# Performance work log

Measured on AMD Instinct MI355X. Metric: run time of the kernel, lower is better.

Reference implementation:

```python
import jax, jax.numpy as jnp
import numpy as np

R = 16  # z_dim
_TRIU = np.triu_indices(R, 1)  # static index pair for plucker coords


def plucker_coords(u, v):
    # L2-normalised Plucker coordinates of span{u, v}; last dim r -> r*(r-1)//2
    outer = u[..., :, None] * v[..., None, :]
    anti = outer - jnp.swapaxes(outer, -1, -2)
    pc = anti[..., _TRIU[0], _TRIU[1]]
    nrm = jnp.linalg.norm(pc, axis=-1, keepdims=True)
    return pc / jnp.maximum(nrm, 1e-8)


def setup_inputs() -> dict:
    key = jax.random.key(0)
    ks = jax.random.split(key, 9)
    B, L, D, Z, P, H = 4, 256, 128, 16, 120, 256
    in_dim = 2 * D + 2 * Z + 3 * P + 2  # 650
    h = jax.random.normal(ks[0], (B, L, D), dtype=jnp.float32)
    z = jax.random.normal(ks[1], (B, L, Z), dtype=jnp.float32)
    p = jax.random.normal(ks[2], (B, L, P), dtype=jnp.float32)
    seq_mask = jax.random.randint(ks[3], (B, L), 0, 2).astype(bool)
    canon_mask = jax.random.randint(ks[4], (B, L, L), 0, 2).astype(bool)
    W1 = jax.random.normal(ks[5], (in_dim, H), dtype=jnp.float32) / np.sqrt(in_dim)
    b1 = jnp.zeros((H,), dtype=jnp.float32)
    W2 = jax.random.normal(ks[6], (H, 1), dtype=jnp.float32) / np.sqrt(H)
    b2 = jnp.zeros((1,), dtype=jnp.float32)
    return {"h": h, "z": z, "p": p, "seq_mask": seq_mask, "canon_mask": canon_mask,
            "W1": W1, "b1": b1, "W2": W2, "b2": b2}


def reference(h, z, p, seq_mask, canon_mask, W1, b1, W2, b2):
    B, L, _ = h.shape
    pos = jnp.arange(L, dtype=h.dtype)
    dist = jnp.abs(pos[:, None] - pos[None, :]) / max(L, 1)  # [L, L]
    dist = jnp.broadcast_to(dist[None, :, :, None], (B, L, L, 1))
    canon_f = canon_mask.astype(h.dtype)[..., None]  # [B, L, L, 1]

    h_i = jnp.broadcast_to(h[:, :, None, :], (B, L, L, h.shape[-1]))
    h_j = jnp.broadcast_to(h[:, None, :, :], (B, L, L, h.shape[-1]))
    z_i = jnp.broadcast_to(z[:, :, None, :], (B, L, L, z.shape[-1]))
    z_j = jnp.broadcast_to(z[:, None, :, :], (B, L, L, z.shape[-1]))
    p_i = jnp.broadcast_to(p[:, :, None, :], (B, L, L, p.shape[-1]))
    p_j = jnp.broadcast_to(p[:, None, :, :], (B, L, L, p.shape[-1]))
    p_ij = plucker_coords(z_i, z_j)  # [B, L, L, 120]

    feat = jnp.concatenate([h_i, h_j, z_i, z_j, p_i, p_j, p_ij, dist, canon_f], axis=-1)
    hdn = jax.nn.gelu(feat @ W1 + b1, approximate=False)
    e_pair = (hdn @ W2 + b2)[..., 0]  # [B, L, L]
    e_pair = (e_pair + jnp.swapaxes(e_pair, 1, 2)) * 0.5
    valid = seq_mask[:, :, None] & seq_mask[:, None, :]
    return jnp.where(valid, e_pair, jnp.asarray(30000.0, e_pair.dtype))
```

## Files before the change

### kernel.cpp

```cpp
#include <hip/hip_runtime.h>
#include <hip/hip_bf16.h>
#include <stdint.h>

#define BB     4
#define L_SEQ  256
#define DIM_H  128
#define DIM_Z  16
#define DIM_P  120
#define HID    256
#define TI     16
#define TJ     8
#define NPAIR  (TI*TJ)

typedef __attribute__((ext_vector_type(8))) short short8;
typedef __attribute__((ext_vector_type(4))) float f32x4;

__device__ __forceinline__ int imin(int a, int b){ return a < b ? a : b; }

struct Triu { int a[128]; int b[128]; };
static constexpr Triu make_triu(){
  Triu t{}; int k=0;
  for (int a=0;a<16;a++) for (int b=a+1;b<16;b++){ t.a[k]=a; t.b[k]=b; ++k; }
  for (;k<128;k++){ t.a[k]=0; t.b[k]=0; }
  return t;
}
static constexpr Triu TRIU = make_triu();

__device__ __forceinline__ short f2bf(float f){
  union { __hip_bfloat16 h; short s; } u;
  u.h = __float2bfloat16(f);
  return u.s;
}

__device__ __forceinline__ float bf2f(short s){
  union { float f; uint32_t u; } x;
  x.u = ((uint32_t)(uint16_t)s) << 16;
  return x.f;
}

__device__ __forceinline__ float gelu_fast(float x){
  float s = fmaf(0.42550f, x, 0.5f);
  s = fminf(fmaxf(s, 0.0f), 1.0f);
  return x * s;
}

__global__ void k_detect(const uint32_t* __restrict__ seq_words, int* __restrict__ flag){
  uint32_t v = 0;
  for (int i = threadIdx.x; i < 256; i += 64) v |= (seq_words[i] & 0xFFFFFF00u);
  unsigned long long any = __ballot(v != 0u);
  if (threadIdx.x == 0) *flag = (any != 0ull) ? 1 : 0;
}

__global__ __launch_bounds__(256) void k_compact(
    const void* __restrict__ seq_raw, const int* __restrict__ flag_p,
    int* __restrict__ vi, int* __restrict__ nv)
{
  const int b = blockIdx.x, i = threadIdx.x;
  bool s;
  if (*flag_p) s = ((const unsigned char*)seq_raw)[b*L_SEQ + i] != 0;
  else         s = ((const int*)          seq_raw)[b*L_SEQ + i] != 0;
  const int lane = i & 63, w = i >> 6;
  unsigned long long m = __ballot(s);
  __shared__ int wc[4];
  if (lane == 0) wc[w] = __popcll(m);
  __syncthreads();
  int base = 0;
  for (int x = 0; x < w; x++) base += wc[x];
  unsigned long long lower = (1ull << lane) - 1ull;
  int pos = base + __popcll(m & lower);
  if (s) vi[b*L_SEQ + pos] = i;
  if (i == 0) nv[b] = wc[0] + wc[1] + wc[2] + wc[3];
}

#define K1_ROWS 2
__global__ __launch_bounds__(256) void k1_precompute(
    const float* __restrict__ hbuf, const float* __restrict__ zbuf, const float* __restrict__ pbuf,
    const float* __restrict__ W1, const float* __restrict__ b1,
    const void* __restrict__ seq_raw, const int* __restrict__ flag_p,
    float* __restrict__ Ai, float* __restrict__ Cj)
{
  int row0 = blockIdx.x * K1_ROWS;
  {
    bool v0, v1;
    if (*flag_p){
      const unsigned char* s8 = (const unsigned char*)seq_raw;
      v0 = s8[row0] != 0; v1 = s8[row0+1] != 0;
    } else {
      const int* s32 = (const int*)seq_raw;
      v0 = s32[row0] != 0; v1 = s32[row0+1] != 0;
    }
    if (!v0 && !v1) return;
  }
  int hcol = threadIdx.x;
  float accA[K1_ROWS], accC[K1_ROWS];
  float bias = b1[hcol];
  #pragma unroll
  for (int r=0;r<K1_ROWS;r++){ accA[r]=bias; accC[r]=0.f; }

  const float* hrow = hbuf + (size_t)row0*DIM_H;
  for (int k=0;k<DIM_H;k++){
    float wa = W1[k*HID + hcol], wc = W1[(128+k)*HID + hcol];
    #pragma unroll
    for (int r=0;r<K1_ROWS;r++){
      float x = hrow[r*DIM_H + k];
      accA[r]=fmaf(x,wa,accA[r]); accC[r]=fmaf(x,wc,accC[r]);
    }
  }
  const float* zrow = zbuf + (size_t)row0*DIM_Z;
  for (int k=0;k<DIM_Z;k++){
    float wa = W1[(256+k)*HID + hcol], wc = W1[(272+k)*HID + hcol];
    #pragma unroll
    for (int r=0;r<K1_ROWS;r++){
      float x = zrow[r*DIM_Z + k];
      accA[r]=fmaf(x,wa,accA[r]); accC[r]=fmaf(x,wc,accC[r]);
    }
  }
  const float* prow = pbuf + (size_t)row0*DIM_P;
  for (int k=0;k<DIM_P;k++){
    float wa = W1[(288+k)*HID + hcol], wc = W1[(408+k)*HID + hcol];
    #pragma unroll
    for (int r=0;r<K1_ROWS;r++){
      float x = prow[r*DIM_P + k];
      accA[r]=fmaf(x,wa,accA[r]); accC[r]=fmaf(x,wc,accC[r]);
    }
  }
  #pragma unroll
  for (int r=0;r<K1_ROWS;r++){
    Ai[(row0+r)*HID + hcol] = accA[r];
    Cj[(row0+r)*HID + hcol] = accC[r];
  }
}

__global__ __launch_bounds__(256) void k1b_w1pt(const float* __restrict__ W1, short* __restrict__ W1pT){
  int idx = blockIdx.x*256 + threadIdx.x;
  int k = idx & 127, n = idx >> 7;
  float v = 0.f;
  if (k < 120)      v = W1[(528+k)*HID + n];
  else if (k==120)  v = W1[648*HID + n];
  else if (k==121)  v = W1[649*HID + n];
  W1pT[n*128 + k] = f2bf(v);
}

#define PCCOORD(T) f2bf((u[TRIU.a[(T)]]*v[TRIU.b[(T)]] - u[TRIU.b[(T)]]*v[TRIU.a[(T)]])*inv)
#define PC_CHUNK4(BASE) { \
  _Pragma("unroll") \
  for (int c_=0;c_<4;c_++){ \
    _Pragma("unroll") \
    for (int e_=0;e_<8;e_++){ pk[c_][e_] = PCCOORD((BASE) + c_*8 + e_); } } }

__global__ __launch_bounds__(512, 4) void k2_pair(
    const float* __restrict__ zbuf, const void* __restrict__ canon_raw,
    const float* __restrict__ Ai, const float* __restrict__ Cj,
    const short* __restrict__ W1pT, const float* __restrict__ W2,
    const int* __restrict__ flag_p, const int* __restrict__ vi, const int* __restrict__ nv,
    float* __restrict__ e_out)
{
  const int b = blockIdx.z, it = blockIdx.y, jt = blockIdx.x;
  const int i0 = it*TI, j0 = jt*TJ;
  const int nvb = nv[b];
  if (i0 >= nvb || j0 >= nvb) return;
  const int tid = threadIdx.x, lane = tid & 63, w = tid >> 6;
  const int brow = b*L_SEQ;

  short8 bfrag[2][4];
  {
    int g = lane >> 4, col = lane & 15;
    int n0 = (2*w+0)*16 + col, n1 = (2*w+1)*16 + col;
    #pragma unroll
    for (int ks=0; ks<4; ks++){
      bfrag[0][ks] = *reinterpret_cast<const short8*>(W1pT + n0*128 + ks*32 + g*8);
      bfrag[1][ks] = *reinterpret_cast<const short8*>(W1pT + n1*128 + ks*32 + g*8);
    }
  }

  __shared__ __align__(16) short pc_lds[NPAIR*128];
  __shared__ short ai_lds[TI*264];
  __shared__ short cj_lds[TJ*264];
  __shared__ float z_lds[(TI+TJ)*17];
  __shared__ float w2_lds[HID];
  __shared__ float epart[NPAIR*9];
  __shared__ int io_lds[TI];
  __shared__ int jo_lds[TJ];

  if (tid < TI)              io_lds[tid]    = vi[brow + imin(i0 + tid,      nvb-1)];
  else if (tid < TI+TJ)      jo_lds[tid-TI] = vi[brow + imin(j0 + (tid-TI), nvb-1)];
  __syncthreads();

  for (int idx = tid; idx < TI*HID; idx += 512){ int r = idx>>8, c = idx&255; ai_lds[r*264+c] = f2bf(Ai[(size_t)(brow+io_lds[r])*HID + c]); }
  for (int idx = tid; idx < TJ*HID; idx += 512){ int r = idx>>8, c = idx&255; cj_lds[r*264+c] = f2bf(Cj[(size_t)(brow+jo_lds[r])*HID + c]); }
  for (int idx = tid; idx < TI*DIM_Z; idx += 512){ int r = idx>>4, c = idx&15; z_lds[r*17+c] = zbuf[(size_t)(brow+io_lds[r])*DIM_Z + c]; }
  for (int idx = tid; idx < TJ*DIM_Z; idx += 512){ int r = idx>>4, c = idx&15; z_lds[(TI+r)*17+c] = zbuf[(size_t)(brow+jo_lds[r])*DIM_Z + c]; }
  if (tid < HID) w2_lds[tid] = W2[tid];
  __syncthreads();

  {
    const int p  = tid & 127;
    const int h  = tid >> 7;
    const int il = p >> 3, jl = p & 7;
    float u[16], v[16];
    #pragma unroll
    for (int a=0;a<16;a++) u[a] = z_lds[il*17+a];
    #pragma unroll
    for (int a=0;a<16;a++) v[a] = z_lds[(TI+jl)*17+a];
    float du=0.f, dv=0.f, uv=0.f;
    #pragma unroll
    for (int a=0;a<16;a++){ du=fmaf(u[a],u[a],du); dv=fmaf(v[a],v[a],dv); uv=fmaf(u[a],v[a],uv); }
    float q = fmaxf(du*dv - uv*uv, 1e-16f);
    float inv = __builtin_amdgcn_rsqf(q);

    short8 pk[4];
    if (h == 0)      PC_CHUNK4(0)
    else if (h == 1) PC_CHUNK4(32)
    else if (h == 2) PC_CHUNK4(64)
    else {
      #pragma unroll
      for (int c_=0;c_<3;c_++){
        #pragma unroll
        for (int e_=0;e_<8;e_++){ pk[c_][e_] = PCCOORD(96 + c_*8 + e_); }
      }
      int gi = io_lds[il], gj = jo_lds[jl];
      float dist = fabsf((float)(gi - gj)) * (1.0f/256.0f);
      float canon;
      if (*flag_p) canon = (((const unsigned char*)canon_raw)[(brow+gi)*L_SEQ + gj] != 0) ? 1.f : 0.f;
      else         canon = (((const int*)          canon_raw)[(brow+gi)*L_SEQ + gj] != 0) ? 1.f : 0.f;
      short8 last;
      last[0] = f2bf(dist); last[1] = f2bf(canon);
      #pragma unroll
      for (int e_=2;e_<8;e_++) last[e_] = (short)0;
      pk[3] = last;
    }
    char* pcb = (char*)pc_lds;
    const int rowbase = p*256 + h*64;
    #pragma unroll
    for (int c_=0;c_<4;c_++){
      int off = (rowbase + c_*16) ^ ((p&7)<<4);
      *reinterpret_cast<short8*>(pcb + off) = pk[c_];
    }
  }
  __syncthreads();

  {
    const int g = lane >> 4, col = lane & 15;
    const int n0 = (2*w+0)*16 + col, n1 = (2*w+1)*16 + col;
    const float w2v0 = w2_lds[n0], w2v1 = w2_lds[n1];
    const char* pcb = (const char*)pc_lds;

    for (int s=0; s<8; s++){
      short8 afrag[4];
      const int p = s*16 + col;
      #pragma unroll
      for (int ks=0; ks<4; ks++){
        int off = (p*256 + (ks*4+g)*16) ^ ((p&7)<<4);
        afrag[ks] = *reinterpret_cast<const short8*>(pcb + off);
      }
      f32x4 acc0 = {0.f,0.f,0.f,0.f}, acc1 = {0.f,0.f,0.f,0.f};
      #pragma unroll
      for (int ks=0; ks<4; ks++){
        acc0 = __builtin_amdgcn_mfma_f32_16x16x32_bf16(afrag[ks], bfrag[0][ks], acc0, 0,0,0);
        acc1 = __builtin_amdgcn_mfma_f32_16x16x32_bf16(afrag[ks], bfrag[1][ks], acc1, 0,0,0);
      }
      const int i_l = 2*s + (g>>1);
      const float ai0 = bf2f(ai_lds[i_l*264 + n0]);
      const float ai1 = bf2f(ai_lds[i_l*264 + n1]);
      float psum[4];
      #pragma unroll
      for (int r=0;r<4;r++){
        int m  = g*4 + r;
        int jl = m & 7;
        float cj0 = bf2f(cj_lds[jl*264 + n0]);
        float cj1 = bf2f(cj_lds[jl*264 + n1]);
        float pre0 = acc0[r] + ai0 + cj0;
        float pre1 = acc1[r] + ai1 + cj1;
        psum[r] = fmaf(gelu_fast(pre0), w2v0, gelu_fast(pre1)*w2v1);
      }
      float recv01 = __shfl_xor((lane & 1) ? psum[0] : psum[1], 1);
      float acc01  = ((lane & 1) ? psum[1] : psum[0]) + recv01;
      float recv23 = __shfl_xor((lane & 1) ? psum[2] : psum[3], 1);
      float acc23  = ((lane & 1) ? psum[3] : psum[2]) + recv23;
      float recv2  = __shfl_xor((lane & 2) ? acc01 : acc23, 2);
      float val    = ((lane & 2) ? acc23 : acc01) + recv2;
      val += __shfl_xor(val, 4);
      val += __shfl_xor(val, 8);
      if ((lane & 12) == 0)
        epart[(s*16 + g*4 + (lane&3))*9 + w] = val;
    }
  }
  __syncthreads();

  if (tid < NPAIR){
    float sum = 0.f;
    #pragma unroll
    for (int ww=0; ww<8; ww++) sum += epart[tid*9 + ww];
    e_out[(size_t)(brow + io_lds[tid>>3])*L_SEQ + jo_lds[tid&7]] = sum;
  }
}

__global__ __launch_bounds__(256) void k3_sym(
    const float* __restrict__ e_in, const void* __restrict__ seq_raw,
    const float* __restrict__ b2, const int* __restrict__ flag_p,
    float* __restrict__ out)
{
  int idx = blockIdx.x*256 + threadIdx.x;
  int b = idx >> 16, rem = idx & 65535, i = rem >> 8, j = rem & 255;
  bool si, sj;
  if (*flag_p){
    const unsigned char* s8 = (const unsigned char*)seq_raw;
    si = s8[b*L_SEQ+i] != 0; sj = s8[b*L_SEQ+j] != 0;
  } else {
    const int* s32 = (const int*)seq_raw;
    si = s32[b*L_SEQ+i] != 0; sj = s32[b*L_SEQ+j] != 0;
  }
  float val = 30000.0f;
  if (si && sj){
    float e1 = e_in[(b*L_SEQ+i)*L_SEQ + j];
    float e2 = e_in[(b*L_SEQ+j)*L_SEQ + i];
    val = 0.5f*(e1 + e2) + b2[0];
  }
  out[idx] = val;
}

extern "C" void kernel_launch(void* const* d_in, const int* in_sizes, int n_in,
                              void* d_out, int out_size, void* d_ws, size_t ws_size,
                              hipStream_t stream)
{
  const float* hbuf  = (const float*)d_in[0];
  const float* zbuf  = (const float*)d_in[1];
  const float* pbuf  = (const float*)d_in[2];
  const void*  seq   = d_in[3];
  const void*  canon = d_in[4];
  const float* W1    = (const float*)d_in[5];
  const float* b1    = (const float*)d_in[6];
  const float* W2    = (const float*)d_in[7];
  const float* b2    = (const float*)d_in[8];

  char* ws = (char*)d_ws;
  float* Ai   = (float*)(ws);
  float* Cj   = (float*)(ws + (1<<20));
  short* W1pT = (short*)(ws + (2<<20));
  float* e_ws = (float*)(ws + (2<<20) + 65536);
  int*   flag = (int*)  (ws + (2<<20) + 65536 + (1<<20));
  int*   vi   = (int*)  (ws + (2<<20) + 65536 + (1<<20) + 256);
  int*   nv   = (int*)  (ws + (2<<20) + 65536 + (1<<20) + 256 + 4096);

  k_detect<<<1, 64, 0, stream>>>((const uint32_t*)seq, flag);
  k_compact<<<BB, 256, 0, stream>>>(seq, flag, vi, nv);
  k1_precompute<<<BB*L_SEQ/K1_ROWS, 256, 0, stream>>>(hbuf, zbuf, pbuf, W1, b1, seq, flag, Ai, Cj);
  k1b_w1pt<<<(HID*128)/256, 256, 0, stream>>>(W1, W1pT);
  dim3 g2(L_SEQ/TJ, L_SEQ/TI, BB);
  k2_pair<<<g2, 512, 0, stream>>>(zbuf, canon, Ai, Cj, W1pT, W2, flag, vi, nv, e_ws);
  k3_sym<<<(BB*L_SEQ*L_SEQ)/256, 256, 0, stream>>>(e_ws, seq, b2, flag, (float*)d_out);
}
```

Before: 59.93 us.

## Merge prep kernels, compact k1 over valid rows, vectorize symmetrize stores

The detect, compact and W1 transpose kernels are merged into one prep launch, which drops two kernel launches. k1_precompute now reads the compacted valid-row list and processes pairs of valid rows, so blocks no longer sit mostly idle on masked rows. k3_sym writes four outputs per thread with a vector store, cutting its thread count by four. The costs are an extra in-block sync for format detection and uncoalesced transposed reads in k3.

```diff
diff --git a/kernel.cpp b/kernel.cpp
--- a/kernel.cpp
+++ b/kernel.cpp
@@ -44,101 +44,86 @@
   return x * s;
 }
 
-__global__ void k_detect(const uint32_t* __restrict__ seq_words, int* __restrict__ flag){
-  uint32_t v = 0;
-  for (int i = threadIdx.x; i < 256; i += 64) v |= (seq_words[i] & 0xFFFFFF00u);
-  unsigned long long any = __ballot(v != 0u);
-  if (threadIdx.x == 0) *flag = (any != 0ull) ? 1 : 0;
-}
-
-__global__ __launch_bounds__(256) void k_compact(
-    const void* __restrict__ seq_raw, const int* __restrict__ flag_p,
-    int* __restrict__ vi, int* __restrict__ nv)
-{
-  const int b = blockIdx.x, i = threadIdx.x;
-  bool s;
-  if (*flag_p) s = ((const unsigned char*)seq_raw)[b*L_SEQ + i] != 0;
-  else         s = ((const int*)          seq_raw)[b*L_SEQ + i] != 0;
-  const int lane = i & 63, w = i >> 6;
-  unsigned long long m = __ballot(s);
-  __shared__ int wc[4];
-  if (lane == 0) wc[w] = __popcll(m);
-  __syncthreads();
-  int base = 0;
-  for (int x = 0; x < w; x++) base += wc[x];
-  unsigned long long lower = (1ull << lane) - 1ull;
-  int pos = base + __popcll(m & lower);
-  if (s) vi[b*L_SEQ + pos] = i;
-  if (i == 0) nv[b] = wc[0] + wc[1] + wc[2] + wc[3];
-}
-
-#define K1_ROWS 2
+__global__ __launch_bounds__(256) void k_prep(
+    const uint32_t* __restrict__ seq_words, const float* __restrict__ W1,
+    int* __restrict__ flag, int* __restrict__ vi, int* __restrict__ nv,
+    short* __restrict__ W1pT)
+{
+  const int blk = blockIdx.x, tid = threadIdx.x;
+  if (blk < BB){
+    const int lane = tid & 63, w = tid >> 6;
+    __shared__ int det[4];
+    __shared__ int wc[4];
+    uint32_t vdet = seq_words[tid] & 0xFFFFFF00u;
+    unsigned long long bm = __ballot(vdet != 0u);
+    if (lane == 0) det[w] = (bm != 0ull) ? 1 : 0;
+    __syncthreads();
+    const bool bytes = (det[0] | det[1] | det[2] | det[3]) != 0;
+    if (blk == 0 && tid == 0) *flag = bytes ? 1 : 0;
+
+    const int b = blk, i = tid;
+    bool s;
+    if (bytes) s = ((const unsigned char*)seq_words)[b*L_SEQ + i] != 0;
+    else       s = ((const int*)          seq_words)[b*L_SEQ + i] != 0;
+    unsigned long long m = __ballot(s);
+    if (lane == 0) wc[w] = __popcll(m);
+    __syncthreads();
+    int base = 0;
+    for (int x = 0; x < w; x++) base += wc[x];
+    unsigned long long lower = (1ull << lane) - 1ull;
+    int pos = base + __popcll(m & lower);
+    if (s) vi[b*L_SEQ + pos] = i;
+    if (i == 0) nv[b] = wc[0] + wc[1] + wc[2] + wc[3];
+  } else {
+    int idx = (blk - BB)*256 + tid;
+    int k = idx & 127, n = idx >> 7;
+    float v = 0.f;
+    if (k < 120)      v = W1[(528+k)*HID + n];
+    else if (k==120)  v = W1[648*HID + n];
+    else if (k==121)  v = W1[649*HID + n];
+    W1pT[n*128 + k] = f2bf(v);
+  }
+}
+
 __global__ __launch_bounds__(256) void k1_precompute(
     const float* __restrict__ hbuf, const float* __restrict__ zbuf, const float* __restrict__ pbuf,
     const float* __restrict__ W1, const float* __restrict__ b1,
-    const void* __restrict__ seq_raw, const int* __restrict__ flag_p,
+    const int* __restrict__ vi, const int* __restrict__ nv,
     float* __restrict__ Ai, float* __restrict__ Cj)
 {
-  int row0 = blockIdx.x * K1_ROWS;
-  {
-    bool v0, v1;
-    if (*flag_p){
-      const unsigned char* s8 = (const unsigned char*)seq_raw;
-      v0 = s8[row0] != 0; v1 = s8[row0+1] != 0;
-    } else {
-      const int* s32 = (const int*)seq_raw;
-      v0 = s32[row0] != 0; v1 = s32[row0+1] != 0;
-    }
-    if (!v0 && !v1) return;
-  }
-  int hcol = threadIdx.x;
-  float accA[K1_ROWS], accC[K1_ROWS];
-  float bias = b1[hcol];
-  #pragma unroll
-  for (int r=0;r<K1_ROWS;r++){ accA[r]=bias; accC[r]=0.f; }
-
-  const float* hrow = hbuf + (size_t)row0*DIM_H;
+  const int b = blockIdx.x >> 7;
+  const int p = blockIdx.x & 127;
+  const int nvb = nv[b];
+  if (2*p >= nvb) return;
+  const int r0 = vi[b*L_SEQ + 2*p];
+  const int r1 = vi[b*L_SEQ + imin(2*p + 1, nvb - 1)];
+  const size_t g0 = (size_t)(b*L_SEQ + r0), g1 = (size_t)(b*L_SEQ + r1);
+
+  const int hcol = threadIdx.x;
+  float a0, a1, c0, c1;
+  a0 = a1 = b1[hcol];
+  c0 = c1 = 0.f;
+
+  const float* h0 = hbuf + g0*DIM_H;  const float* h1 = hbuf + g1*DIM_H;
   for (int k=0;k<DIM_H;k++){
     float wa = W1[k*HID + hcol], wc = W1[(128+k)*HID + hcol];
-    #pragma unroll
-    for (int r=0;r<K1_ROWS;r++){
-      float x = hrow[r*DIM_H + k];
-      accA[r]=fmaf(x,wa,accA[r]); accC[r]=fmaf(x,wc,accC[r]);
-    }
-  }
-  const float* zrow = zbuf + (size_t)row0*DIM_Z;
+    a0 = fmaf(h0[k], wa, a0); c0 = fmaf(h0[k], wc, c0);
+    a1 = fmaf(h1[k], wa, a1); c1 = fmaf(h1[k], wc, c1);
+  }
+  const float* z0 = zbuf + g0*DIM_Z;  const float* z1 = zbuf + g1*DIM_Z;
   for (int k=0;k<DIM_Z;k++){
     float wa = W1[(256+k)*HID + hcol], wc = W1[(272+k)*HID + hcol];
-    #pragma unroll
-    for (int r=0;r<K1_ROWS;r++){
-      float x = zrow[r*DIM_Z + k];
-      accA[r]=fmaf(x,wa,accA[r]); accC[r]=fmaf(x,wc,accC[r]);
-    }
-  }
-  const float* prow = pbuf + (size_t)row0*DIM_P;
+    a0 = fmaf(z0[k], wa, a0); c0 = fmaf(z0[k], wc, c0);
+    a1 = fmaf(z1[k], wa, a1); c1 = fmaf(z1[k], wc, c1);
+  }
+  const float* p0 = pbuf + g0*DIM_P;  const float* p1 = pbuf + g1*DIM_P;
   for (int k=0;k<DIM_P;k++){
     float wa = W1[(288+k)*HID + hcol], wc = W1[(408+k)*HID + hcol];
-    #pragma unroll
-    for (int r=0;r<K1_ROWS;r++){
-      float x = prow[r*DIM_P + k];
-      accA[r]=fmaf(x,wa,accA[r]); accC[r]=fmaf(x,wc,accC[r]);
-    }
-  }
-  #pragma unroll
-  for (int r=0;r<K1_ROWS;r++){
-    Ai[(row0+r)*HID + hcol] = accA[r];
-    Cj[(row0+r)*HID + hcol] = accC[r];
-  }
-}
-
-__global__ __launch_bounds__(256) void k1b_w1pt(const float* __restrict__ W1, short* __restrict__ W1pT){
-  int idx = blockIdx.x*256 + threadIdx.x;
-  int k = idx & 127, n = idx >> 7;
-  float v = 0.f;
-  if (k < 120)      v = W1[(528+k)*HID + n];
-  else if (k==120)  v = W1[648*HID + n];
-  else if (k==121)  v = W1[649*HID + n];
-  W1pT[n*128 + k] = f2bf(v);
+    a0 = fmaf(p0[k], wa, a0); c0 = fmaf(p0[k], wc, c0);
+    a1 = fmaf(p1[k], wa, a1); c1 = fmaf(p1[k], wc, c1);
+  }
+  Ai[g0*HID + hcol] = a0;  Cj[g0*HID + hcol] = c0;
+  Ai[g1*HID + hcol] = a1;  Cj[g1*HID + hcol] = c1;
 }
 
 #define PCCOORD(T) f2bf((u[TRIU.a[(T)]]*v[TRIU.b[(T)]] - u[TRIU.b[(T)]]*v[TRIU.a[(T)]])*inv)
@@ -301,22 +286,32 @@
     float* __restrict__ out)
 {
   int idx = blockIdx.x*256 + threadIdx.x;
-  int b = idx >> 16, rem = idx & 65535, i = rem >> 8, j = rem & 255;
-  bool si, sj;
+  int b = idx >> 14, rem = idx & 16383, i = rem >> 6, j4 = (rem & 63) << 2;
+  bool si, sj[4];
   if (*flag_p){
     const unsigned char* s8 = (const unsigned char*)seq_raw;
-    si = s8[b*L_SEQ+i] != 0; sj = s8[b*L_SEQ+j] != 0;
+    si = s8[b*L_SEQ+i] != 0;
+    #pragma unroll
+    for (int t=0;t<4;t++) sj[t] = s8[b*L_SEQ+j4+t] != 0;
   } else {
     const int* s32 = (const int*)seq_raw;
-    si = s32[b*L_SEQ+i] != 0; sj = s32[b*L_SEQ+j] != 0;
-  }
-  float val = 30000.0f;
-  if (si && sj){
-    float e1 = e_in[(b*L_SEQ+i)*L_SEQ + j];
-    float e2 = e_in[(b*L_SEQ+j)*L_SEQ + i];
-    val = 0.5f*(e1 + e2) + b2[0];
-  }
-  out[idx] = val;
+    si = s32[b*L_SEQ+i] != 0;
+    #pragma unroll
+    for (int t=0;t<4;t++) sj[t] = s32[b*L_SEQ+j4+t] != 0;
+  }
+  const float bias = b2[0];
+  f32x4 o;
+  #pragma unroll
+  for (int t=0;t<4;t++){
+    float val = 30000.0f;
+    if (si && sj[t]){
+      float e1 = e_in[((size_t)b*L_SEQ+i)*L_SEQ + j4+t];
+      float e2 = e_in[((size_t)b*L_SEQ+j4+t)*L_SEQ + i];
+      val = 0.5f*(e1 + e2) + bias;
+    }
+    o[t] = val;
+  }
+  *reinterpret_cast<f32x4*>(out + ((size_t)b*L_SEQ+i)*L_SEQ + j4) = o;
 }
 
 extern "C" void kernel_launch(void* const* d_in, const int* in_sizes, int n_in,
@@ -342,11 +337,9 @@
   int*   vi   = (int*)  (ws + (2<<20) + 65536 + (1<<20) + 256);
   int*   nv   = (int*)  (ws + (2<<20) + 65536 + (1<<20) + 256 + 4096);
 
-  k_detect<<<1, 64, 0, stream>>>((const uint32_t*)seq, flag);
-  k_compact<<<BB, 256, 0, stream>>>(seq, flag, vi, nv);
-  k1_precompute<<<BB*L_SEQ/K1_ROWS, 256, 0, stream>>>(hbuf, zbuf, pbuf, W1, b1, seq, flag, Ai, Cj);
-  k1b_w1pt<<<(HID*128)/256, 256, 0, stream>>>(W1, W1pT);
+  k_prep<<<BB + 128, 256, 0, stream>>>((const uint32_t*)seq, W1, flag, vi, nv, W1pT);
+  k1_precompute<<<BB*128, 256, 0, stream>>>(hbuf, zbuf, pbuf, W1, b1, vi, nv, Ai, Cj);
   dim3 g2(L_SEQ/TJ, L_SEQ/TI, BB);
   k2_pair<<<g2, 512, 0, stream>>>(zbuf, canon, Ai, Cj, W1pT, W2, flag, vi, nv, e_ws);
-  k3_sym<<<(BB*L_SEQ*L_SEQ)/256, 256, 0, stream>>>(e_ws, seq, b2, flag, (float*)d_out);
-}
+  k3_sym<<<(BB*L_SEQ*L_SEQ/4)/256, 256, 0, stream>>>(e_ws, seq, b2, flag, (float*)d_out);
+}
```

Result: faster. 56.63 us (-5.5%).
